# Optimization experiments

Hardware: AMD Instinct MI355X
Metric: run time of the kernel (lower is better)

Reference implementation:

```python
import jax, jax.numpy as jnp
import numpy as np

D_MODEL = 1024
N_HEADS = 16
HEAD_DIM = D_MODEL // N_HEADS
B, S = 2, 2048


def setup_inputs() -> dict:
    key = jax.random.key(0)
    ks = jax.random.split(key, 10)
    q = jax.random.normal(ks[0], (B, S, D_MODEL), dtype=jnp.float32)
    k = jax.random.normal(ks[1], (B, S, D_MODEL), dtype=jnp.float32)
    v = jax.random.normal(ks[2], (B, S, D_MODEL), dtype=jnp.float32)
    # causal mask: 1 where attention is forbidden (upper triangle), 0 elsewhere
    mask = jnp.triu(jnp.ones((S, S), dtype=jnp.float32), k=1)[None, None, :, :]
    scale = 0.02
    Wk = jax.random.normal(ks[3], (D_MODEL, D_MODEL), dtype=jnp.float32) * scale
    bk = jnp.zeros((D_MODEL,), dtype=jnp.float32)
    Wv = jax.random.normal(ks[4], (D_MODEL, D_MODEL), dtype=jnp.float32) * scale
    bv = jnp.zeros((D_MODEL,), dtype=jnp.float32)
    Wo = jax.random.normal(ks[5], (D_MODEL, D_MODEL), dtype=jnp.float32) * scale
    bo = jnp.zeros((D_MODEL,), dtype=jnp.float32)
    return {"query": q, "key": k, "value": v, "mask": mask,
            "Wk": Wk, "bk": bk, "Wv": Wv, "bv": bv, "Wo": Wo, "bo": bo}


def reference(query, key, value, mask, Wk, bk, Wv, bv, Wo, bo):
    b, s, d = query.shape
    h, dh = N_HEADS, HEAD_DIM

    def split(x):  # [b, s, d] -> [b, h, s, dh]
        return x.reshape(b, -1, h, dh).transpose(0, 2, 1, 3)

    # NOTE: faithful to source bug — query is projected with weights_key.
    q = split(query @ Wk.T + bk)
    k = split(key @ Wk.T + bk)
    v = split(value @ Wv.T + bv)

    inv_sqrt_dh = jnp.float32(1.0 / np.sqrt(dh))
    scores = jnp.einsum('bhqd,bhkd->bhqk', q, k) * inv_sqrt_dh
    scores = scores + mask * jnp.float32(-1e9)
    w = jax.nn.softmax(scores, axis=-1)           # [b, h, s, s]
    ctx = jnp.einsum('bhqk,bhkd->bhqd', w, v)     # [b, h, s, dh]
    concat = ctx.transpose(0, 2, 1, 3).reshape(b, -1, d)
    out = concat @ Wo.T + bo
    return (out, w)
```

## Files before the change

kernel.cpp:

```cpp
#include <hip/hip_runtime.h>
#include <stdint.h>

#define BB 2
#define SS 2048
#define DD 1024
#define HH 16
#define DH 64
#define MM 4096

typedef unsigned short u16;
typedef __attribute__((ext_vector_type(8))) __bf16 bf16x8;
typedef __attribute__((ext_vector_type(4))) float f32x4;

__device__ __forceinline__ u16 f2bf(float f) {
    union { float f; unsigned int u; } x; x.f = f;
    unsigned int u = x.u;
    return (u16)((u + 0x7fffu + ((u >> 16) & 1u)) >> 16);
}

__device__ __forceinline__ float bf2f(u16 u) {
    union { unsigned int u; float f; } x; x.u = ((unsigned int)u) << 16;
    return x.f;
}

__device__ __forceinline__ void gl_lds16(const u16* g, u16* l) {
    __builtin_amdgcn_global_load_lds(
        (const __attribute__((address_space(1))) unsigned int*)g,
        (__attribute__((address_space(3))) unsigned int*)l, 16, 0, 0);
}

__global__ __launch_bounds__(256) void cvt_all_kernel(
    const float* __restrict__ q, const float* __restrict__ k, const float* __restrict__ v,
    const float* __restrict__ wk, const float* __restrict__ wv, const float* __restrict__ wo,
    u16* __restrict__ Xq, u16* __restrict__ Xk, u16* __restrict__ Xv,
    u16* __restrict__ Wkb, u16* __restrict__ Wvb, u16* __restrict__ Wob) {
    int i = blockIdx.x * 256 + threadIdx.x;
    const float* s; u16* d; int off;
    if (i < 1048576)      { s = q;  d = Xq;  off = i; }
    else if (i < 2097152) { s = k;  d = Xk;  off = i - 1048576; }
    else if (i < 3145728) { s = v;  d = Xv;  off = i - 2097152; }
    else if (i < 3407872) { s = wk; d = Wkb; off = i - 3145728; }
    else if (i < 3670016) { s = wv; d = Wvb; off = i - 3407872; }
    else                  { s = wo; d = Wob; off = i - 3670016; }
    float4 val = ((const float4*)s)[off];
    ushort4 o;
    o.x = f2bf(val.x); o.y = f2bf(val.y); o.z = f2bf(val.z); o.w = f2bf(val.w);
    ((ushort4*)d)[off] = o;
}

template <int OUT_MODE>
__device__ __forceinline__ void gemm_core(u16* As, u16* Bs,
                                          const u16* __restrict__ A,
                                          const u16* __restrict__ W,
                                          const float* __restrict__ bias,
                                          void* __restrict__ Cout,
                                          int bx, int by) {
    const int tid = threadIdx.x;
    const int lane = tid & 63, wid = tid >> 6;
    const int wy = wid >> 1, wx = wid & 1;
    const int quad = lane >> 4, cl = lane & 15;
    const int m0 = by * 128, n0 = bx * 128;

    f32x4 acc[4][4];
#pragma unroll
    for (int i = 0; i < 4; ++i)
#pragma unroll
        for (int j = 0; j < 4; ++j) acc[i][j] = (f32x4){0.f, 0.f, 0.f, 0.f};

    const int ch0 = tid;
    const int row0 = ch0 >> 2, ko0 = (ch0 & 3) * 8;
    const int ch1 = 256 + tid;
    const int row1 = ch1 >> 2, ko1 = (ch1 & 3) * 8;
    const int lb0 = (wid * 64) * 8;
    const int lb1 = (256 + wid * 64) * 8;

    for (int kt = 0; kt < 1024; kt += 32) {
        __syncthreads();
        gl_lds16(A + (size_t)(m0 + row0) * 1024 + kt + ko0, As + lb0);
        gl_lds16(W + (size_t)(n0 + row0) * 1024 + kt + ko0, Bs + lb0);
        gl_lds16(A + (size_t)(m0 + row1) * 1024 + kt + ko1, As + lb1);
        gl_lds16(W + (size_t)(n0 + row1) * 1024 + kt + ko1, Bs + lb1);
        __syncthreads();
        bf16x8 af[4], bfr[4];
#pragma unroll
        for (int t = 0; t < 4; ++t) {
            af[t]  = *(const bf16x8*)(As + (wy * 64 + t * 16 + cl) * 32 + quad * 8);
            bfr[t] = *(const bf16x8*)(Bs + (wx * 64 + t * 16 + cl) * 32 + quad * 8);
        }
#pragma unroll
        for (int mt = 0; mt < 4; ++mt)
#pragma unroll
            for (int nt = 0; nt < 4; ++nt)
                acc[mt][nt] = __builtin_amdgcn_mfma_f32_16x16x32_bf16(
                    af[mt], bfr[nt], acc[mt][nt], 0, 0, 0);
    }

#pragma unroll
    for (int mt = 0; mt < 4; ++mt) {
#pragma unroll
        for (int nt = 0; nt < 4; ++nt) {
            int n = n0 + wx * 64 + nt * 16 + cl;
            float bv = bias[n];
#pragma unroll
            for (int r = 0; r < 4; ++r) {
                int m = m0 + wy * 64 + mt * 16 + quad * 4 + r;
                float v = acc[mt][nt][r] + bv;
                if (OUT_MODE == 0) {
                    int b = m >> 11, s = m & 2047, h = n >> 6, d = n & 63;
                    ((u16*)Cout)[((size_t)(b * 16 + h) * 2048 + s) * 64 + d] = f2bf(v);
                } else if (OUT_MODE == 1) {
                    int b = m >> 11, s = m & 2047, h = n >> 6, d = n & 63;
                    ((u16*)Cout)[((size_t)(b * 16 + h) * 64 + d) * 2048 + s] = f2bf(v);
                } else {
                    ((float*)Cout)[(size_t)m * 1024 + n] = v;
                }
            }
        }
    }
}

__global__ __launch_bounds__(256, 2) void proj_kernel(
    const u16* __restrict__ Xq, const u16* __restrict__ Xk, const u16* __restrict__ Xv,
    const u16* __restrict__ Wkb, const u16* __restrict__ Wvb,
    const float* __restrict__ bk, const float* __restrict__ bv,
    u16* __restrict__ Qh, u16* __restrict__ Kh, u16* __restrict__ Vt) {
    __shared__ u16 As[128 * 32];
    __shared__ u16 Bs[128 * 32];
    int z = blockIdx.z;
    const u16* A = (z == 0) ? Xq : (z == 1) ? Xk : Xv;
    const u16* W = (z == 2) ? Wvb : Wkb;
    const float* bias = (z == 2) ? bv : bk;
    if (z == 2)
        gemm_core<1>(As, Bs, A, W, bias, Vt, blockIdx.x, blockIdx.y);
    else
        gemm_core<0>(As, Bs, A, W, bias, (z == 0) ? (void*)Qh : (void*)Kh,
                     blockIdx.x, blockIdx.y);
}

__global__ __launch_bounds__(256, 2) void outproj_kernel(
    const u16* __restrict__ Ctx, const u16* __restrict__ Wob,
    const float* __restrict__ bo, float* __restrict__ out) {
    __shared__ u16 As[128 * 32];
    __shared__ u16 Bs[128 * 32];
    gemm_core<2>(As, Bs, Ctx, Wob, bo, out, blockIdx.x, blockIdx.y);
}

__global__ __launch_bounds__(256, 2) void attn_kernel(
    const u16* __restrict__ Qh, const u16* __restrict__ Kh, const u16* __restrict__ Vt,
    float* __restrict__ Wout, u16* __restrict__ Ctx) {
    __shared__ u16 Ks[64 * 72];
    __shared__ u16 Vs[64 * 72];
    __shared__ u16 Ps[128 * 72];
    __shared__ float rlS[128];

    const int tid = threadIdx.x;
    const int lane = tid & 63, wid = tid >> 6;
    const int quad = lane >> 4, cl = lane & 15;
    const int bh = blockIdx.y;
    const int qb = ((bh >> 4) & 1) ? (15 - (int)blockIdx.x) : (int)blockIdx.x;
    const int q0 = qb * 128;
    const int b = bh >> 4, h = bh & 15;

    const u16* Qp = Qh + (size_t)bh * 2048 * 64;
    const u16* Kp = Kh + (size_t)bh * 2048 * 64;
    const u16* Vp = Vt + (size_t)bh * 64 * 2048;
    float* Wp = Wout + (size_t)bh * 2048 * 2048;

    bf16x8 qf[2][2];
#pragma unroll
    for (int mt = 0; mt < 2; ++mt)
#pragma unroll
        for (int ks = 0; ks < 2; ++ks) {
            int row = q0 + wid * 32 + mt * 16 + cl;
            qf[mt][ks] = *(const bf16x8*)(Qp + (size_t)row * 64 + ks * 32 + quad * 8);
        }

    float lsum[8];
#pragma unroll
    for (int i = 0; i < 8; ++i) lsum[i] = 0.f;

    const int nkt = 2 * qb + 2;

    for (int kt = 0; kt < nkt; ++kt) {
        __syncthreads();
#pragma unroll
        for (int j = 0; j < 2; ++j) {
            int ch = j * 256 + tid;
            int row = ch >> 3, ko = (ch & 7) * 8;
            *(uint4*)(Ks + row * 72 + ko) =
                *(const uint4*)(Kp + (size_t)(kt * 64 + row) * 64 + ko);
        }
        __syncthreads();

        const bool tile_masked = (kt >= 2 * qb);
        f32x4 sc[2][4];
#pragma unroll
        for (int nt = 0; nt < 4; ++nt) {
            bf16x8 kf0 = *(const bf16x8*)(Ks + (nt * 16 + cl) * 72 + quad * 8);
            bf16x8 kf1 = *(const bf16x8*)(Ks + (nt * 16 + cl) * 72 + 32 + quad * 8);
#pragma unroll
            for (int mt = 0; mt < 2; ++mt) {
                f32x4 a = (f32x4){0.f, 0.f, 0.f, 0.f};
                a = __builtin_amdgcn_mfma_f32_16x16x32_bf16(qf[mt][0], kf0, a, 0, 0, 0);
                a = __builtin_amdgcn_mfma_f32_16x16x32_bf16(qf[mt][1], kf1, a, 0, 0, 0);
                sc[mt][nt] = a;
            }
        }
#pragma unroll
        for (int mt = 0; mt < 2; ++mt)
#pragma unroll
            for (int r = 0; r < 4; ++r) {
                int li = mt * 4 + r;
                int grow = q0 + wid * 32 + mt * 16 + quad * 4 + r;
                float acc = 0.f;
#pragma unroll
                for (int nt = 0; nt < 4; ++nt) {
                    int gcol = kt * 64 + nt * 16 + cl;
                    float p = __expf(sc[mt][nt][r] * 0.125f);
                    if (tile_masked) p = (gcol <= grow) ? p : 0.f;
                    acc += p;
                }
                lsum[li] += acc;
            }
    }

    float rli[8];
#pragma unroll
    for (int i = 0; i < 8; ++i) {
        float s = lsum[i];
#pragma unroll
        for (int off = 1; off < 16; off <<= 1) s += __shfl_xor(s, off);
        rli[i] = 1.0f / s;
    }
    if (cl == 0) {
#pragma unroll
        for (int mt = 0; mt < 2; ++mt)
#pragma unroll
            for (int r = 0; r < 4; ++r)
                rlS[wid * 32 + mt * 16 + quad * 4 + r] = rli[mt * 4 + r];
    }

    f32x4 ctx[2][4];
#pragma unroll
    for (int mt = 0; mt < 2; ++mt)
#pragma unroll
        for (int d = 0; d < 4; ++d) ctx[mt][d] = (f32x4){0.f, 0.f, 0.f, 0.f};

    for (int kt = 0; kt < nkt; ++kt) {
        __syncthreads();
#pragma unroll
        for (int j = 0; j < 2; ++j) {
            int ch = j * 256 + tid;
            int row = ch >> 3, ko = (ch & 7) * 8;
            *(uint4*)(Ks + row * 72 + ko) =
                *(const uint4*)(Kp + (size_t)(kt * 64 + row) * 64 + ko);
            *(uint4*)(Vs + row * 72 + ko) =
                *(const uint4*)(Vp + (size_t)row * 2048 + kt * 64 + ko);
        }
        __syncthreads();

        const bool tile_masked = (kt >= 2 * qb);
        f32x4 sc[2][4];
#pragma unroll
        for (int nt = 0; nt < 4; ++nt) {
            bf16x8 kf0 = *(const bf16x8*)(Ks + (nt * 16 + cl) * 72 + quad * 8);
            bf16x8 kf1 = *(const bf16x8*)(Ks + (nt * 16 + cl) * 72 + 32 + quad * 8);
#pragma unroll
            for (int mt = 0; mt < 2; ++mt) {
                f32x4 a = (f32x4){0.f, 0.f, 0.f, 0.f};
                a = __builtin_amdgcn_mfma_f32_16x16x32_bf16(qf[mt][0], kf0, a, 0, 0, 0);
                a = __builtin_amdgcn_mfma_f32_16x16x32_bf16(qf[mt][1], kf1, a, 0, 0, 0);
                sc[mt][nt] = a;
            }
        }
#pragma unroll
        for (int mt = 0; mt < 2; ++mt)
#pragma unroll
            for (int r = 0; r < 4; ++r) {
                int lrow = wid * 32 + mt * 16 + quad * 4 + r;
                int grow = q0 + lrow;
#pragma unroll
                for (int nt = 0; nt < 4; ++nt) {
                    int gcol = kt * 64 + nt * 16 + cl;
                    float p = __expf(sc[mt][nt][r] * 0.125f);
                    if (tile_masked) p = (gcol <= grow) ? p : 0.f;
                    Ps[lrow * 72 + nt * 16 + cl] = f2bf(p);
                }
            }
        __syncthreads();

#pragma unroll
        for (int c = 0; c < 8; ++c) {
            int idx = c * 256 + tid;
            int row = idx >> 4, q4 = idx & 15;
            const u16* pw = Ps + row * 72 + q4 * 4;
            float rl = rlS[row];
            f32x4 o;
            o[0] = bf2f(pw[0]) * rl; o[1] = bf2f(pw[1]) * rl;
            o[2] = bf2f(pw[2]) * rl; o[3] = bf2f(pw[3]) * rl;
            __builtin_nontemporal_store(
                o, (f32x4*)(Wp + (size_t)(q0 + row) * 2048 + kt * 64 + q4 * 4));
        }

#pragma unroll
        for (int ks = 0; ks < 2; ++ks) {
            bf16x8 pf[2];
#pragma unroll
            for (int mt = 0; mt < 2; ++mt)
                pf[mt] = *(const bf16x8*)(Ps + (wid * 32 + mt * 16 + cl) * 72 + ks * 32 + quad * 8);
#pragma unroll
            for (int d = 0; d < 4; ++d) {
                bf16x8 vf = *(const bf16x8*)(Vs + (d * 16 + cl) * 72 + ks * 32 + quad * 8);
#pragma unroll
                for (int mt = 0; mt < 2; ++mt)
                    ctx[mt][d] = __builtin_amdgcn_mfma_f32_16x16x32_bf16(
                        pf[mt], vf, ctx[mt][d], 0, 0, 0);
            }
        }
    }

    for (int zt = qb + 1; zt < 16; ++zt) {
        f32x4 z = (f32x4){0.f, 0.f, 0.f, 0.f};
#pragma unroll
        for (int j = 0; j < 16; ++j) {
            int idx = j * 256 + tid;
            int row = idx >> 5, col4 = idx & 31;
            __builtin_nontemporal_store(
                z, (f32x4*)(Wp + (size_t)(q0 + row) * 2048 + zt * 128 + col4 * 4));
        }
    }

#pragma unroll
    for (int mt = 0; mt < 2; ++mt)
#pragma unroll
        for (int d = 0; d < 4; ++d)
#pragma unroll
            for (int r = 0; r < 4; ++r) {
                int li = mt * 4 + r;
                int grow = q0 + wid * 32 + mt * 16 + quad * 4 + r;
                int col = d * 16 + cl;
                float v = ctx[mt][d][r] * rli[li];
                Ctx[((size_t)(b * 2048 + grow)) * 1024 + h * 64 + col] = f2bf(v);
            }
}

extern "C" void kernel_launch(void* const* d_in, const int* in_sizes, int n_in,
                              void* d_out, int out_size, void* d_ws, size_t ws_size,
                              hipStream_t stream) {
    const float* qin = (const float*)d_in[0];
    const float* kin = (const float*)d_in[1];
    const float* vin = (const float*)d_in[2];
    const float* Wk = (const float*)d_in[4];
    const float* bk = (const float*)d_in[5];
    const float* Wv = (const float*)d_in[6];
    const float* bv = (const float*)d_in[7];
    const float* Wo = (const float*)d_in[8];
    const float* bo = (const float*)d_in[9];

    float* outp = (float*)d_out;
    float* wout = outp + (size_t)MM * DD;

    u16* Xq  = (u16*)d_ws;
    u16* Xk  = Xq  + (size_t)MM * DD;
    u16* Xv  = Xk  + (size_t)MM * DD;
    u16* Wkb = Xv  + (size_t)MM * DD;
    u16* Wvb = Wkb + (size_t)DD * DD;
    u16* Wob = Wvb + (size_t)DD * DD;
    u16* Qh  = Wob + (size_t)DD * DD;
    u16* Kh  = Qh  + (size_t)MM * DD;
    u16* Vt  = Kh  + (size_t)MM * DD;
    u16* Ctx = Vt  + (size_t)MM * DD;

    dim3 blk(256, 1, 1);
    cvt_all_kernel<<<dim3(15360, 1, 1), blk, 0, stream>>>(
        qin, kin, vin, Wk, Wv, Wo, Xq, Xk, Xv, Wkb, Wvb, Wob);
    proj_kernel<<<dim3(8, 32, 3), blk, 0, stream>>>(Xq, Xk, Xv, Wkb, Wvb, bk, bv, Qh, Kh, Vt);
    attn_kernel<<<dim3(16, 32, 1), blk, 0, stream>>>(Qh, Kh, Vt, wout, Ctx);
    outproj_kernel<<<dim3(8, 32, 1), blk, 0, stream>>>(Ctx, Wob, bo, outp);
}
```

Measured before the change: 739.3 us.

## Read K/V fragments directly from global, drop block barriers, remap block order

Removes the shared-memory staging of K and V tiles and every __syncthreads in the attention loops, so each wave loads its MFMA fragments straight from global memory (relying on L1/L2 reuse) and uses only wave-local Ps rows. The normalized weight matrix is now written per element straight from registers instead of through a vectorized pass over shared memory, and the 1/sqrt(dh) scale is folded into Q at load time. The block-to-(bh, q-tile) mapping is also permuted to interleave heads and balance causal work. This risks more global load traffic, uncoalesced scalar stores of the large weights output, and an extra bf16 rounding of the scaled Q.

```diff
diff --git a/kernel.cpp b/kernel.cpp
--- a/kernel.cpp
+++ b/kernel.cpp
@@ -148,16 +148,16 @@
 __global__ __launch_bounds__(256, 2) void attn_kernel(
     const u16* __restrict__ Qh, const u16* __restrict__ Kh, const u16* __restrict__ Vt,
     float* __restrict__ Wout, u16* __restrict__ Ctx) {
-    __shared__ u16 Ks[64 * 72];
-    __shared__ u16 Vs[64 * 72];
     __shared__ u16 Ps[128 * 72];
-    __shared__ float rlS[128];
 
     const int tid = threadIdx.x;
     const int lane = tid & 63, wid = tid >> 6;
     const int quad = lane >> 4, cl = lane & 15;
-    const int bh = blockIdx.y;
-    const int qb = ((bh >> 4) & 1) ? (15 - (int)blockIdx.x) : (int)blockIdx.x;
+
+    const int linear = (int)blockIdx.x + ((int)blockIdx.y << 4);
+    const int bh = ((linear & 7) << 2) | ((linear >> 3) & 3);
+    const int v0_ = (linear >> 5) & 15;
+    const int qb = (v0_ < 8) ? v0_ : 23 - v0_;
     const int q0 = qb * 128;
     const int b = bh >> 4, h = bh & 15;
 
@@ -172,7 +172,12 @@
 #pragma unroll
         for (int ks = 0; ks < 2; ++ks) {
             int row = q0 + wid * 32 + mt * 16 + cl;
-            qf[mt][ks] = *(const bf16x8*)(Qp + (size_t)row * 64 + ks * 32 + quad * 8);
+            bf16x8 raw = *(const bf16x8*)(Qp + (size_t)row * 64 + ks * 32 + quad * 8);
+            const u16* rw = (const u16*)&raw;
+            u16 out8[8];
+#pragma unroll
+            for (int e = 0; e < 8; ++e) out8[e] = f2bf(bf2f(rw[e]) * 0.125f);
+            qf[mt][ks] = *(const bf16x8*)out8;
         }
 
     float lsum[8];
@@ -182,22 +187,13 @@
     const int nkt = 2 * qb + 2;
 
     for (int kt = 0; kt < nkt; ++kt) {
-        __syncthreads();
-#pragma unroll
-        for (int j = 0; j < 2; ++j) {
-            int ch = j * 256 + tid;
-            int row = ch >> 3, ko = (ch & 7) * 8;
-            *(uint4*)(Ks + row * 72 + ko) =
-                *(const uint4*)(Kp + (size_t)(kt * 64 + row) * 64 + ko);
-        }
-        __syncthreads();
-
         const bool tile_masked = (kt >= 2 * qb);
         f32x4 sc[2][4];
 #pragma unroll
         for (int nt = 0; nt < 4; ++nt) {
-            bf16x8 kf0 = *(const bf16x8*)(Ks + (nt * 16 + cl) * 72 + quad * 8);
-            bf16x8 kf1 = *(const bf16x8*)(Ks + (nt * 16 + cl) * 72 + 32 + quad * 8);
+            const u16* kr = Kp + (size_t)(kt * 64 + nt * 16 + cl) * 64 + quad * 8;
+            bf16x8 kf0 = *(const bf16x8*)kr;
+            bf16x8 kf1 = *(const bf16x8*)(kr + 32);
 #pragma unroll
             for (int mt = 0; mt < 2; ++mt) {
                 f32x4 a = (f32x4){0.f, 0.f, 0.f, 0.f};
@@ -216,7 +212,7 @@
 #pragma unroll
                 for (int nt = 0; nt < 4; ++nt) {
                     int gcol = kt * 64 + nt * 16 + cl;
-                    float p = __expf(sc[mt][nt][r] * 0.125f);
+                    float p = __expf(sc[mt][nt][r]);
                     if (tile_masked) p = (gcol <= grow) ? p : 0.f;
                     acc += p;
                 }
@@ -232,13 +228,6 @@
         for (int off = 1; off < 16; off <<= 1) s += __shfl_xor(s, off);
         rli[i] = 1.0f / s;
     }
-    if (cl == 0) {
-#pragma unroll
-        for (int mt = 0; mt < 2; ++mt)
-#pragma unroll
-            for (int r = 0; r < 4; ++r)
-                rlS[wid * 32 + mt * 16 + quad * 4 + r] = rli[mt * 4 + r];
-    }
 
     f32x4 ctx[2][4];
 #pragma unroll
@@ -247,24 +236,13 @@
         for (int d = 0; d < 4; ++d) ctx[mt][d] = (f32x4){0.f, 0.f, 0.f, 0.f};
 
     for (int kt = 0; kt < nkt; ++kt) {
-        __syncthreads();
-#pragma unroll
-        for (int j = 0; j < 2; ++j) {
-            int ch = j * 256 + tid;
-            int row = ch >> 3, ko = (ch & 7) * 8;
-            *(uint4*)(Ks + row * 72 + ko) =
-                *(const uint4*)(Kp + (size_t)(kt * 64 + row) * 64 + ko);
-            *(uint4*)(Vs + row * 72 + ko) =
-                *(const uint4*)(Vp + (size_t)row * 2048 + kt * 64 + ko);
-        }
-        __syncthreads();
-
         const bool tile_masked = (kt >= 2 * qb);
         f32x4 sc[2][4];
 #pragma unroll
         for (int nt = 0; nt < 4; ++nt) {
-            bf16x8 kf0 = *(const bf16x8*)(Ks + (nt * 16 + cl) * 72 + quad * 8);
-            bf16x8 kf1 = *(const bf16x8*)(Ks + (nt * 16 + cl) * 72 + 32 + quad * 8);
+            const u16* kr = Kp + (size_t)(kt * 64 + nt * 16 + cl) * 64 + quad * 8;
+            bf16x8 kf0 = *(const bf16x8*)kr;
+            bf16x8 kf1 = *(const bf16x8*)(kr + 32);
 #pragma unroll
             for (int mt = 0; mt < 2; ++mt) {
                 f32x4 a = (f32x4){0.f, 0.f, 0.f, 0.f};
@@ -277,30 +255,20 @@
         for (int mt = 0; mt < 2; ++mt)
 #pragma unroll
             for (int r = 0; r < 4; ++r) {
+                int li = mt * 4 + r;
                 int lrow = wid * 32 + mt * 16 + quad * 4 + r;
                 int grow = q0 + lrow;
+                float rl = rli[li];
 #pragma unroll
                 for (int nt = 0; nt < 4; ++nt) {
                     int gcol = kt * 64 + nt * 16 + cl;
-                    float p = __expf(sc[mt][nt][r] * 0.125f);
+                    float p = __expf(sc[mt][nt][r]);
                     if (tile_masked) p = (gcol <= grow) ? p : 0.f;
+                    __builtin_nontemporal_store(p * rl, Wp + (size_t)grow * 2048 + gcol);
                     Ps[lrow * 72 + nt * 16 + cl] = f2bf(p);
                 }
             }
-        __syncthreads();
-
-#pragma unroll
-        for (int c = 0; c < 8; ++c) {
-            int idx = c * 256 + tid;
-            int row = idx >> 4, q4 = idx & 15;
-            const u16* pw = Ps + row * 72 + q4 * 4;
-            float rl = rlS[row];
-            f32x4 o;
-            o[0] = bf2f(pw[0]) * rl; o[1] = bf2f(pw[1]) * rl;
-            o[2] = bf2f(pw[2]) * rl; o[3] = bf2f(pw[3]) * rl;
-            __builtin_nontemporal_store(
-                o, (f32x4*)(Wp + (size_t)(q0 + row) * 2048 + kt * 64 + q4 * 4));
-        }
+        asm volatile("s_waitcnt lgkmcnt(0)" ::: "memory");
 
 #pragma unroll
         for (int ks = 0; ks < 2; ++ks) {
@@ -310,7 +278,8 @@
                 pf[mt] = *(const bf16x8*)(Ps + (wid * 32 + mt * 16 + cl) * 72 + ks * 32 + quad * 8);
 #pragma unroll
             for (int d = 0; d < 4; ++d) {
-                bf16x8 vf = *(const bf16x8*)(Vs + (d * 16 + cl) * 72 + ks * 32 + quad * 8);
+                bf16x8 vf = *(const bf16x8*)(Vp + (size_t)(d * 16 + cl) * 2048 +
+                                             kt * 64 + ks * 32 + quad * 8);
 #pragma unroll
                 for (int mt = 0; mt < 2; ++mt)
                     ctx[mt][d] = __builtin_amdgcn_mfma_f32_16x16x32_bf16(
```

Measured after the change: 779.5 us. +5.4%, slower.
